# Kernel tuning notes

Measured on AMD Instinct MI355X. Metric: run time of the kernel, lower is better.

The kernel has to match this reference:

```python
import jax, jax.numpy as jnp
import numpy as np

INPUT_SIZE = 1024
HIDDEN = 2048
B = 4096


def setup_inputs() -> dict:
    key = jax.random.key(0)
    ks = jax.random.split(key, 11)
    D = INPUT_SIZE + HIDDEN
    bound = 1.0 / np.sqrt(D)  # nn.Linear default init range
    def lin(kw, kb):
        W = jax.random.uniform(kw, (HIDDEN, D), jnp.float32, -bound, bound)
        b = jax.random.uniform(kb, (HIDDEN,), jnp.float32, -bound, bound)
        return W, b
    W_i, b_i = lin(ks[0], ks[1])
    W_f, b_f = lin(ks[2], ks[3])
    W_c, b_c = lin(ks[4], ks[5])
    W_o, b_o = lin(ks[6], ks[7])
    x_t = jax.random.normal(ks[8], (B, INPUT_SIZE), jnp.float32)
    h_prev = jax.random.normal(ks[9], (B, HIDDEN), jnp.float32)
    c_prev = jax.random.normal(ks[10], (B, HIDDEN), jnp.float32)
    return {
        "x_t": x_t, "h_prev": h_prev, "c_prev": c_prev,
        "W_i": W_i, "b_i": b_i, "W_f": W_f, "b_f": b_f,
        "W_c": W_c, "b_c": b_c, "W_o": W_o, "b_o": b_o,
    }


def reference(x_t, h_prev, c_prev, W_i, b_i, W_f, b_f, W_c, b_c, W_o, b_o):
    # combined: [B, input+hidden]
    combined = jnp.concatenate([x_t, h_prev], axis=1)
    # fused gate GEMM: stack the four weight matrices -> one [D, 4H] matmul
    W_all = jnp.concatenate([W_i, W_f, W_c, W_o], axis=0)  # [4H, D]
    b_all = jnp.concatenate([b_i, b_f, b_c, b_o], axis=0)  # [4H]
    gates = combined @ W_all.T + b_all                     # [B, 4H]
    gi, gf, gc, go = jnp.split(gates, 4, axis=1)
    i_t = jax.nn.sigmoid(gi)
    f_t = jax.nn.sigmoid(gf)
    g_t = jnp.tanh(gc)
    o_t = jax.nn.sigmoid(go)
    c_t = f_t * c_prev + i_t * g_t
    h_t = o_t * jnp.tanh(c_t)
    # dropout is identity in eval / p=0
    return (h_t, c_t)
```

## Files before the change

### kernel.cpp

```cpp
#include <hip/hip_runtime.h>
#include <stdint.h>

#define B_DIM 4096
#define IN_SZ 1024
#define HID   2048
#define D_DIM 3072
#define BM 128
#define BH 32
#define BK 32

typedef float  f32x4  __attribute__((ext_vector_type(4)));
typedef short  short8 __attribute__((ext_vector_type(8)));

__device__ __forceinline__ unsigned short f2bf(float f) {
    union { float f; unsigned u; } v; v.f = f;
    unsigned u = v.u + 0x7fffu + ((v.u >> 16) & 1u);
    return (unsigned short)(u >> 16);
}

__device__ __forceinline__ void async_load16(const void* g, void* l) {
    __builtin_amdgcn_global_load_lds(
        (const __attribute__((address_space(1))) unsigned int*)g,
        (__attribute__((address_space(3))) unsigned int*)l,
        16, 0, 0);
}

__device__ __forceinline__ float sigm(float x) {
    return 1.0f / (1.0f + __expf(-x));
}
__device__ __forceinline__ float tanh_f(float x) {
    return 1.0f - 2.0f / (__expf(2.0f * x) + 1.0f);
}

__global__ void convert_combined(const float* __restrict__ x,
                                 const float* __restrict__ h,
                                 unsigned short* __restrict__ dst) {
    int idx = blockIdx.x * blockDim.x + threadIdx.x;
    const int C4 = D_DIM / 4;
    if (idx >= B_DIM * C4) return;
    int b  = idx / C4;
    int c4 = idx - b * C4;
    float4 v;
    if (c4 < IN_SZ / 4) v = ((const float4*)x)[b * (IN_SZ / 4) + c4];
    else                v = ((const float4*)h)[b * (HID / 4) + (c4 - IN_SZ / 4)];
    ushort4 o;
    o.x = f2bf(v.x); o.y = f2bf(v.y); o.z = f2bf(v.z); o.w = f2bf(v.w);
    ((ushort4*)dst)[idx] = o;
}

__global__ void convert_W(const float* __restrict__ W0, const float* __restrict__ W1,
                          const float* __restrict__ W2, const float* __restrict__ W3,
                          unsigned short* __restrict__ dst) {
    int idx = blockIdx.x * blockDim.x + threadIdx.x;
    const int PG = HID * D_DIM / 4;
    if (idx >= 4 * PG) return;
    int g = idx / PG;
    int r = idx - g * PG;
    const float* W = (g == 0) ? W0 : (g == 1) ? W1 : (g == 2) ? W2 : W3;
    float4 v = ((const float4*)W)[r];
    ushort4 o;
    o.x = f2bf(v.x); o.y = f2bf(v.y); o.z = f2bf(v.z); o.w = f2bf(v.w);
    ((ushort4*)dst)[idx] = o;
}

__global__ __launch_bounds__(256, 2)
void lstm_gemm(const unsigned short* __restrict__ Abf,
               const unsigned short* __restrict__ Wbf,
               const float* __restrict__ b_i, const float* __restrict__ b_f,
               const float* __restrict__ b_c, const float* __restrict__ b_o,
               const float* __restrict__ c_prev,
               float* __restrict__ h_out, float* __restrict__ c_out) {
    __shared__ unsigned short sA[BM * BK];
    __shared__ unsigned short sB[BM * BK];

    const int tid  = threadIdx.x;
    const int lane = tid & 63;
    const int wave = tid >> 6;
    const int l16  = lane & 15;
    const int quad = lane >> 4;

    const int m0 = blockIdx.x * BM;
    const int h0 = blockIdx.y * BH;

    f32x4 acc[2][8] = {};

    const int srow = lane >> 2;
    const int scol = (lane & 3) * 8;
    const unsigned short* gA = Abf + (size_t)(m0 + wave * 32 + srow) * D_DIM + scol;
    const unsigned short* gB = Wbf + (size_t)(wave * HID + h0 + srow) * D_DIM + scol;
    unsigned short* lA0 = &sA[(wave * 32) * BK];
    unsigned short* lA1 = &sA[(wave * 32 + 16) * BK];
    unsigned short* lB0 = &sB[(wave * 32) * BK];
    unsigned short* lB1 = &sB[(wave * 32 + 16) * BK];

    for (int kk = 0; kk < D_DIM / BK; ++kk) {
        const int k0 = kk * BK;
        if (kk) __syncthreads();
        async_load16(gA + k0,                 lA0 + lane * 8);
        async_load16(gA + 16 * D_DIM + k0,    lA1 + lane * 8);
        async_load16(gB + k0,                 lB0 + lane * 8);
        async_load16(gB + 16 * D_DIM + k0,    lB1 + lane * 8);
        __syncthreads();

        short8 a0 = *(const short8*)&sA[(wave * 32 + l16) * BK + quad * 8];
        short8 a1 = *(const short8*)&sA[(wave * 32 + 16 + l16) * BK + quad * 8];
#pragma unroll
        for (int ct = 0; ct < 8; ++ct) {
            short8 b = *(const short8*)&sB[(ct * 16 + l16) * BK + quad * 8];
            acc[0][ct] = __builtin_amdgcn_mfma_f32_16x16x32_bf16(a0, b, acc[0][ct], 0, 0, 0);
            acc[1][ct] = __builtin_amdgcn_mfma_f32_16x16x32_bf16(a1, b, acc[1][ct], 0, 0, 0);
        }
    }

    const int rbase = m0 + wave * 32 + quad * 4;
#pragma unroll
    for (int cj = 0; cj < 2; ++cj) {
        const int h  = h0 + cj * 16 + l16;
        const float bi = b_i[h], bf = b_f[h], bc = b_c[h], bo = b_o[h];
#pragma unroll
        for (int rt = 0; rt < 2; ++rt) {
#pragma unroll
            for (int r = 0; r < 4; ++r) {
                const int m = rbase + rt * 16 + r;
                const size_t off = (size_t)m * HID + h;
                float gi = acc[rt][0 + cj][r] + bi;
                float gf = acc[rt][2 + cj][r] + bf;
                float gc = acc[rt][4 + cj][r] + bc;
                float go = acc[rt][6 + cj][r] + bo;
                float it = sigm(gi);
                float ft = sigm(gf);
                float gt = tanh_f(gc);
                float ot = sigm(go);
                float c  = ft * c_prev[off] + it * gt;
                float hv = ot * tanh_f(c);
                h_out[off] = hv;
                c_out[off] = c;
            }
        }
    }
}

extern "C" void kernel_launch(void* const* d_in, const int* in_sizes, int n_in,
                              void* d_out, int out_size, void* d_ws, size_t ws_size,
                              hipStream_t stream) {
    const float* x_t    = (const float*)d_in[0];
    const float* h_prev = (const float*)d_in[1];
    const float* c_prev = (const float*)d_in[2];
    const float* W_i = (const float*)d_in[3];
    const float* b_i = (const float*)d_in[4];
    const float* W_f = (const float*)d_in[5];
    const float* b_f = (const float*)d_in[6];
    const float* W_c = (const float*)d_in[7];
    const float* b_c = (const float*)d_in[8];
    const float* W_o = (const float*)d_in[9];
    const float* b_o = (const float*)d_in[10];
    float* out = (float*)d_out;

    unsigned short* Abf = (unsigned short*)d_ws;
    unsigned short* Wbf = (unsigned short*)((char*)d_ws + (size_t)B_DIM * D_DIM * 2);

    {
        int n = B_DIM * D_DIM / 4;
        convert_combined<<<(n + 255) / 256, 256, 0, stream>>>(x_t, h_prev, Abf);
    }
    {
        int n = 4 * HID * D_DIM / 4;
        convert_W<<<(n + 255) / 256, 256, 0, stream>>>(W_i, W_f, W_c, W_o, Wbf);
    }
    dim3 grid(B_DIM / BM, HID / BH);
    lstm_gemm<<<grid, 256, 0, stream>>>(Abf, Wbf, b_i, b_f, b_c, b_o, c_prev,
                                        out, out + (size_t)B_DIM * HID);
}
```

Baseline: 465.3 us.

## Rewrite LSTM GEMM with larger swizzled double-buffered tiles and fused conversion

The GEMM kernel is rebuilt around 256x(4x64) tiles with BK=64 and 512 threads arranged as 8 waves. Shared memory is XOR-swizzled and double-buffered with async global-to-LDS prefetch, and MFMA phases are interleaved with setprio and sched barriers. The goal is far more operand reuse per LDS byte and overlap of loads with compute, in place of the old single-buffered 128x32 tile. The two bf16 conversion kernels are merged into one 8-wide kernel, and a 128 KB dynamic LDS allocation is requested. The large LDS footprint likely limits occupancy to one block per CU despite launch_bounds(512,2).

```diff
diff --git a/kernel.cpp b/kernel.cpp
--- a/kernel.cpp
+++ b/kernel.cpp
@@ -5,9 +5,10 @@
 #define IN_SZ 1024
 #define HID   2048
 #define D_DIM 3072
-#define BM 128
-#define BH 32
-#define BK 32
+#define BM 256
+#define BN 64
+#define BK 64
+#define NT (D_DIM / BK)
 
 typedef float  f32x4  __attribute__((ext_vector_type(4)));
 typedef short  short8 __attribute__((ext_vector_type(8)));
@@ -32,110 +33,196 @@
     return 1.0f - 2.0f / (__expf(2.0f * x) + 1.0f);
 }
 
-__global__ void convert_combined(const float* __restrict__ x,
-                                 const float* __restrict__ h,
-                                 unsigned short* __restrict__ dst) {
+__global__ __launch_bounds__(256)
+void convert_all(const float* __restrict__ x, const float* __restrict__ h,
+                 const float* __restrict__ W0, const float* __restrict__ W1,
+                 const float* __restrict__ W2, const float* __restrict__ W3,
+                 unsigned short* __restrict__ Abf, unsigned short* __restrict__ Wbf) {
+    const int NA = B_DIM * D_DIM / 8;
+    const int NW = 4 * HID * D_DIM / 8;
     int idx = blockIdx.x * blockDim.x + threadIdx.x;
-    const int C4 = D_DIM / 4;
-    if (idx >= B_DIM * C4) return;
-    int b  = idx / C4;
-    int c4 = idx - b * C4;
-    float4 v;
-    if (c4 < IN_SZ / 4) v = ((const float4*)x)[b * (IN_SZ / 4) + c4];
-    else                v = ((const float4*)h)[b * (HID / 4) + (c4 - IN_SZ / 4)];
-    ushort4 o;
-    o.x = f2bf(v.x); o.y = f2bf(v.y); o.z = f2bf(v.z); o.w = f2bf(v.w);
-    ((ushort4*)dst)[idx] = o;
-}
-
-__global__ void convert_W(const float* __restrict__ W0, const float* __restrict__ W1,
-                          const float* __restrict__ W2, const float* __restrict__ W3,
-                          unsigned short* __restrict__ dst) {
-    int idx = blockIdx.x * blockDim.x + threadIdx.x;
-    const int PG = HID * D_DIM / 4;
-    if (idx >= 4 * PG) return;
-    int g = idx / PG;
-    int r = idx - g * PG;
-    const float* W = (g == 0) ? W0 : (g == 1) ? W1 : (g == 2) ? W2 : W3;
-    float4 v = ((const float4*)W)[r];
-    ushort4 o;
-    o.x = f2bf(v.x); o.y = f2bf(v.y); o.z = f2bf(v.z); o.w = f2bf(v.w);
-    ((ushort4*)dst)[idx] = o;
-}
-
-__global__ __launch_bounds__(256, 2)
+    const float* src;
+    unsigned short* dst;
+    if (idx < NA) {
+        const int C8 = D_DIM / 8;
+        int b = idx / C8, c8 = idx - b * C8;
+        src = (c8 < IN_SZ / 8) ? x + (size_t)b * IN_SZ + c8 * 8
+                               : h + (size_t)b * HID + (c8 - IN_SZ / 8) * 8;
+        dst = Abf + (size_t)idx * 8;
+    } else {
+        int wi = idx - NA;
+        if (wi >= NW) return;
+        const int PG = HID * D_DIM / 8;
+        int g = wi / PG, r = wi - g * PG;
+        const float* W = (g == 0) ? W0 : (g == 1) ? W1 : (g == 2) ? W2 : W3;
+        src = W + (size_t)r * 8;
+        dst = Wbf + (size_t)wi * 8;
+    }
+    float4 v0 = ((const float4*)src)[0];
+    float4 v1 = ((const float4*)src)[1];
+    short8 o;
+    o[0] = (short)f2bf(v0.x); o[1] = (short)f2bf(v0.y);
+    o[2] = (short)f2bf(v0.z); o[3] = (short)f2bf(v0.w);
+    o[4] = (short)f2bf(v1.x); o[5] = (short)f2bf(v1.y);
+    o[6] = (short)f2bf(v1.z); o[7] = (short)f2bf(v1.w);
+    *(short8*)dst = o;
+}
+
+template <int IB>
+__device__ __forceinline__ void read_a(short8 (&aR)[4][2], const char* smA,
+                                       int aBase, int sw0, int sw1) {
+#pragma unroll
+    for (int i = 0; i < 4; ++i) {
+        aR[i][0] = *(const short8*)(smA + aBase + (IB + i) * 2048 + sw0);
+        aR[i][1] = *(const short8*)(smA + aBase + (IB + i) * 2048 + sw1);
+    }
+}
+
+template <int JB>
+__device__ __forceinline__ void read_b(short8 (&bR)[4][2], const char* smB,
+                                       int bBase, int sw0, int sw1) {
+#pragma unroll
+    for (int j = 0; j < 2; ++j) {
+        bR[JB + j][0] = *(const short8*)(smB + bBase + (JB + j) * 2048 + sw0);
+        bR[JB + j][1] = *(const short8*)(smB + bBase + (JB + j) * 2048 + sw1);
+    }
+}
+
+template <int IB, int JB>
+__device__ __forceinline__ void mfma_quad(f32x4 (&acc)[8][4], const short8 (&aR)[4][2],
+                                          const short8 (&bR)[4][2]) {
+#pragma unroll
+    for (int i = 0; i < 4; ++i)
+#pragma unroll
+        for (int j = 0; j < 2; ++j)
+#pragma unroll
+            for (int s = 0; s < 2; ++s)
+                acc[IB + i][JB + j] = __builtin_amdgcn_mfma_f32_16x16x32_bf16(
+                    aR[i][s], bR[JB + j][s], acc[IB + i][JB + j], 0, 0, 0);
+}
+
+__global__ __launch_bounds__(512, 2)
 void lstm_gemm(const unsigned short* __restrict__ Abf,
                const unsigned short* __restrict__ Wbf,
                const float* __restrict__ b_i, const float* __restrict__ b_f,
                const float* __restrict__ b_c, const float* __restrict__ b_o,
                const float* __restrict__ c_prev,
                float* __restrict__ h_out, float* __restrict__ c_out) {
-    __shared__ unsigned short sA[BM * BK];
-    __shared__ unsigned short sB[BM * BK];
+    extern __shared__ char sm[];
 
     const int tid  = threadIdx.x;
     const int lane = tid & 63;
     const int wave = tid >> 6;
+    const int wm   = wave >> 2;
+    const int wn   = wave & 3;
     const int l16  = lane & 15;
     const int quad = lane >> 4;
+    const int r7   = l16 & 7;
 
     const int m0 = blockIdx.x * BM;
-    const int h0 = blockIdx.y * BH;
-
-    f32x4 acc[2][8] = {};
-
-    const int srow = lane >> 2;
-    const int scol = (lane & 3) * 8;
-    const unsigned short* gA = Abf + (size_t)(m0 + wave * 32 + srow) * D_DIM + scol;
-    const unsigned short* gB = Wbf + (size_t)(wave * HID + h0 + srow) * D_DIM + scol;
-    unsigned short* lA0 = &sA[(wave * 32) * BK];
-    unsigned short* lA1 = &sA[(wave * 32 + 16) * BK];
-    unsigned short* lB0 = &sB[(wave * 32) * BK];
-    unsigned short* lB1 = &sB[(wave * 32 + 16) * BK];
-
-    for (int kk = 0; kk < D_DIM / BK; ++kk) {
-        const int k0 = kk * BK;
-        if (kk) __syncthreads();
-        async_load16(gA + k0,                 lA0 + lane * 8);
-        async_load16(gA + 16 * D_DIM + k0,    lA1 + lane * 8);
-        async_load16(gB + k0,                 lB0 + lane * 8);
-        async_load16(gB + 16 * D_DIM + k0,    lB1 + lane * 8);
-        __syncthreads();
-
-        short8 a0 = *(const short8*)&sA[(wave * 32 + l16) * BK + quad * 8];
-        short8 a1 = *(const short8*)&sA[(wave * 32 + 16 + l16) * BK + quad * 8];
-#pragma unroll
-        for (int ct = 0; ct < 8; ++ct) {
-            short8 b = *(const short8*)&sB[(ct * 16 + l16) * BK + quad * 8];
-            acc[0][ct] = __builtin_amdgcn_mfma_f32_16x16x32_bf16(a0, b, acc[0][ct], 0, 0, 0);
-            acc[1][ct] = __builtin_amdgcn_mfma_f32_16x16x32_bf16(a1, b, acc[1][ct], 0, 0, 0);
+    const int h0 = blockIdx.y * BN;
+
+    const int g8 = lane >> 3;
+    const int sl = (lane & 7) ^ g8;
+    const unsigned short* srcA[4];
+    const unsigned short* srcB[4];
+#pragma unroll
+    for (int i = 0; i < 4; ++i) {
+        const int rt = (wave * 4 + i) * 8 + g8;
+        srcA[i] = Abf + (size_t)(m0 + rt) * D_DIM + sl * 8;
+        const int grow = ((rt >> 4) & 3) * HID + h0 + (rt >> 6) * 16 + (rt & 15);
+        srcB[i] = Wbf + (size_t)grow * D_DIM + sl * 8;
+    }
+    const int chunk = wave * 4096;
+
+    const int aBase = (wm * 128 + l16) * 128;
+    const int bBase = (wn * 64  + l16) * 128;
+    const int sw0 = ((0 * 4 + quad) ^ r7) * 16;
+    const int sw1 = ((1 * 4 + quad) ^ r7) * 16;
+
+    f32x4 acc[8][4] = {};
+    short8 aR[4][2], bR[4][2];
+
+#pragma unroll
+    for (int i = 0; i < 4; ++i) {
+        async_load16(srcA[i], sm + chunk + i * 1024);
+        async_load16(srcB[i], sm + 32768 + chunk + i * 1024);
+    }
+    asm volatile("s_waitcnt vmcnt(0)" ::: "memory");
+    __builtin_amdgcn_s_barrier();
+
+    for (int kt = 0; kt < NT; ++kt) {
+        const char* smA = sm + (kt & 1) * 65536;
+        const char* smB = smA + 32768;
+        char* smAn = sm + ((kt + 1) & 1) * 65536;
+        char* smBn = smAn + 32768;
+        const int koff = (kt + 1) * BK;
+        const bool pf = (kt + 1 < NT);
+
+        if (pf) {
+#pragma unroll
+            for (int i = 0; i < 4; ++i)
+                async_load16(srcA[i] + koff, smAn + chunk + i * 1024);
         }
-    }
-
-    const int rbase = m0 + wave * 32 + quad * 4;
-#pragma unroll
-    for (int cj = 0; cj < 2; ++cj) {
-        const int h  = h0 + cj * 16 + l16;
-        const float bi = b_i[h], bf = b_f[h], bc = b_c[h], bo = b_o[h];
-#pragma unroll
-        for (int rt = 0; rt < 2; ++rt) {
-#pragma unroll
-            for (int r = 0; r < 4; ++r) {
-                const int m = rbase + rt * 16 + r;
-                const size_t off = (size_t)m * HID + h;
-                float gi = acc[rt][0 + cj][r] + bi;
-                float gf = acc[rt][2 + cj][r] + bf;
-                float gc = acc[rt][4 + cj][r] + bc;
-                float go = acc[rt][6 + cj][r] + bo;
-                float it = sigm(gi);
-                float ft = sigm(gf);
-                float gt = tanh_f(gc);
-                float ot = sigm(go);
-                float c  = ft * c_prev[off] + it * gt;
-                float hv = ot * tanh_f(c);
-                h_out[off] = hv;
-                c_out[off] = c;
-            }
+        read_a<0>(aR, smA, aBase, sw0, sw1);
+        read_b<0>(bR, smB, bBase, sw0, sw1);
+        __builtin_amdgcn_s_barrier();
+        asm volatile("s_waitcnt lgkmcnt(0)" ::: "memory");
+        __builtin_amdgcn_sched_barrier(0);
+        __builtin_amdgcn_s_setprio(1);
+        mfma_quad<0, 0>(acc, aR, bR);
+        __builtin_amdgcn_s_setprio(0);
+        __builtin_amdgcn_s_barrier();
+
+        if (pf) {
+#pragma unroll
+            for (int i = 0; i < 4; ++i)
+                async_load16(srcB[i] + koff, smBn + chunk + i * 1024);
+        }
+        read_b<2>(bR, smB, bBase, sw0, sw1);
+        __builtin_amdgcn_s_barrier();
+        asm volatile("s_waitcnt lgkmcnt(0)" ::: "memory");
+        __builtin_amdgcn_sched_barrier(0);
+        __builtin_amdgcn_s_setprio(1);
+        mfma_quad<0, 2>(acc, aR, bR);
+        __builtin_amdgcn_s_setprio(0);
+        __builtin_amdgcn_s_barrier();
+
+        read_a<4>(aR, smA, aBase, sw0, sw1);
+        __builtin_amdgcn_s_barrier();
+        asm volatile("s_waitcnt lgkmcnt(0)" ::: "memory");
+        __builtin_amdgcn_sched_barrier(0);
+        __builtin_amdgcn_s_setprio(1);
+        mfma_quad<4, 2>(acc, aR, bR);
+        __builtin_amdgcn_s_setprio(0);
+        __builtin_amdgcn_s_barrier();
+
+        __builtin_amdgcn_sched_barrier(0);
+        __builtin_amdgcn_s_setprio(1);
+        mfma_quad<4, 0>(acc, aR, bR);
+        __builtin_amdgcn_s_setprio(0);
+        asm volatile("s_waitcnt vmcnt(0)" ::: "memory");
+        __builtin_amdgcn_s_barrier();
+    }
+
+    const int h = h0 + wn * 16 + l16;
+    const float biv = b_i[h], bfv = b_f[h], bcv = b_c[h], bov = b_o[h];
+    const int mb = m0 + wm * 128 + quad * 4;
+#pragma unroll
+    for (int i = 0; i < 8; ++i) {
+#pragma unroll
+        for (int r = 0; r < 4; ++r) {
+            const int m = mb + i * 16 + r;
+            const size_t off = (size_t)m * HID + h;
+            const float gi = acc[i][0][r] + biv;
+            const float gf = acc[i][1][r] + bfv;
+            const float gc = acc[i][2][r] + bcv;
+            const float go = acc[i][3][r] + bov;
+            const float it = sigm(gi), ft = sigm(gf);
+            const float gt = tanh_f(gc), ot = sigm(go);
+            const float c = ft * c_prev[off] + it * gt;
+            h_out[off] = ot * tanh_f(c);
+            c_out[off] = c;
         }
     }
 }
@@ -159,15 +246,19 @@
     unsigned short* Abf = (unsigned short*)d_ws;
     unsigned short* Wbf = (unsigned short*)((char*)d_ws + (size_t)B_DIM * D_DIM * 2);
 
+    static bool s_attr = false;
+    if (!s_attr) {
+        (void)hipFuncSetAttribute((const void*)lstm_gemm,
+                                  hipFuncAttributeMaxDynamicSharedMemorySize, 131072);
+        s_attr = true;
+    }
+
     {
-        int n = B_DIM * D_DIM / 4;
-        convert_combined<<<(n + 255) / 256, 256, 0, stream>>>(x_t, h_prev, Abf);
-    }
-    {
-        int n = 4 * HID * D_DIM / 4;
-        convert_W<<<(n + 255) / 256, 256, 0, stream>>>(W_i, W_f, W_c, W_o, Wbf);
-    }
-    dim3 grid(B_DIM / BM, HID / BH);
-    lstm_gemm<<<grid, 256, 0, stream>>>(Abf, Wbf, b_i, b_f, b_c, b_o, c_prev,
-                                        out, out + (size_t)B_DIM * HID);
-}
+        const int n = (B_DIM * D_DIM + 4 * HID * D_DIM) / 8;
+        convert_all<<<n / 256, 256, 0, stream>>>(x_t, h_prev, W_i, W_f, W_c, W_o,
+                                                 Abf, Wbf);
+    }
+    dim3 grid(B_DIM / BM, HID / BN);
+    lstm_gemm<<<grid, 512, 131072, stream>>>(Abf, Wbf, b_i, b_f, b_c, b_o, c_prev,
+                                             out, out + (size_t)B_DIM * HID);
+}
```

After: 387.3 us. -16.8%, faster.
